# Optimization experiments

Hardware: AMD Instinct MI355X
Metric: run time of the kernel (lower is better)

The kernel has to match this reference:

```python
import jax, jax.numpy as jnp
import numpy as np

T, E, B, D, N = 4, 4096, 2, 128, 384


def setup_inputs() -> dict:
    key = jax.random.key(0)
    ks = jax.random.split(key, 8)
    x = jax.random.normal(ks[0], (T, E, B, D), jnp.float32)
    feats = jax.random.normal(ks[1], (N, N, B, D), jnp.float32)
    # Node ids in [1, N]; id 0 is the padding row/col of the (N+1,N+1) grid.
    # Shared edge list across the batch (matches the repo's usage: the torch
    # scatter broadcasts one value over all batch slots, which is only
    # self-consistent when nodes are identical across batch).
    nodes1 = jax.random.randint(ks[2], (1, E, 2), 1, N + 1)
    nodes = jnp.broadcast_to(nodes1, (B, E, 2)).astype(jnp.int32)
    padding_mask = jnp.zeros((B, E), bool)
    padding_mask_feats = jnp.zeros((B, N), bool)
    pad = jax.random.normal(ks[3], (1,), jnp.float32)
    s1 = 1.0 / np.sqrt(D)
    s2 = 1.0 / np.sqrt(2 * D)
    W_g = jax.random.normal(ks[4], (D, D), jnp.float32) * s1
    b_g = jnp.zeros((D,), jnp.float32)
    W_lin = jax.random.normal(ks[5], (D, 2 * D), jnp.float32) * s2
    b_lin = jnp.zeros((D,), jnp.float32)
    W_f = jax.random.normal(ks[6], (D, D), jnp.float32) * s1
    b_f = jnp.zeros((D,), jnp.float32)
    return dict(x=x, feats=feats, nodes=nodes, padding_mask=padding_mask,
                padding_mask_feats=padding_mask_feats, pad=pad,
                W_g=W_g, b_g=b_g, W_lin=W_lin, b_lin=b_lin, W_f=W_f, b_f=b_f)


def _forward(x, feats, nodes, pad, W_g, b_g, W_lin, b_lin, W_f, b_f):
    # graph_layer stand-in: dense projection over embed dim
    x = jnp.einsum('tebd,od->tebo', x, W_g) + b_g            # (T,E,B,D)
    n_nodes, _, bsz, dim = feats.shape
    xmean = x.mean(0)                                        # (E,B,D)
    # dense padded (N+1,N+1,B,D) grid filled with learned pad value (faithful)
    grid = jnp.ones((n_nodes + 1, n_nodes + 1, bsz, dim), x.dtype) * pad
    n0 = nodes[0, :, 0]                                      # (E,) shared graph
    n1 = nodes[0, :, 1]
    grid = grid.at[n0, n1].set(xmean)                        # scatter edges into grid
    feats_update = grid[1:, 1:]                              # drop pad row/col -> (N,N,B,D)
    cat = jnp.concatenate([feats, feats_update], axis=-1)    # (N,N,B,2D)
    feats = jnp.einsum('nmbc,oc->nmbo', cat, W_lin) + b_lin  # Linear(2D -> D)
    # feat_layer stand-in: dense projection
    feats = jnp.einsum('nmbd,od->nmbo', feats, W_f) + b_f
    nodes_0 = jnp.maximum(nodes - 1, 0)                      # clamp after -1 shift
    g0 = nodes_0[:, :, 0].T                                  # (E,B)
    g1 = nodes_0[:, :, 1].T
    bidx = jnp.arange(bsz)[None, :]                          # (1,B)
    feats_subset = feats[g0, g1, bidx]                       # gather -> (E,B,D)
    x = x + feats_subset[None]                               # broadcast over trials
    return x, feats


def reference(x, feats, nodes, padding_mask, padding_mask_feats, pad,
              W_g, b_g, W_lin, b_lin, W_f, b_f):
    # padding masks are accepted for signature parity; the stub sub-layers
    # (single linear projections) do not consume them.
    return _forward(x, feats, nodes, pad, W_g, b_g, W_lin, b_lin, W_f, b_f)
```

## Files before the change

### kernel.cpp

```cpp
#include <hip/hip_runtime.h>
#include <hip/hip_bf16.h>


constexpr int T_ = 4, E_ = 4096, B_ = 2, D_ = 128, N_ = 384;
constexpr int EB = E_ * B_;
constexpr int XSTRIDE_T = E_ * B_ * D_;
constexpr int XROWS = T_ * EB;
constexpr int NROWS = N_ * N_ * B_;
constexpr int NCELLS = N_ * N_;

typedef __attribute__((ext_vector_type(8))) short bf16x8;
typedef __attribute__((ext_vector_type(4))) float f32x4;
union BF8 { bf16x8 v; ushort u[8]; };

constexpr size_t OFF_WTG    = 0;
constexpr size_t OFF_WTL    = 16384;
constexpr size_t OFF_WTR    = 32768;
constexpr size_t OFF_BCOMB  = 49152;
constexpr size_t OFF_BP     = 49280;
constexpr size_t OFF_XMEAN  = 49408;
constexpr size_t OFF_UC     = OFF_XMEAN + (size_t)EB * D_;
constexpr size_t OFF_WIN    = OFF_UC + (size_t)EB * D_;
constexpr size_t OFF_BPACK  = OFF_WIN + (size_t)NCELLS;
constexpr size_t OFF_BPACKG = OFF_BPACK + 16384;
constexpr size_t OFF_BPACKR = OFF_BPACKG + 16384;
constexpr size_t OFF_WGR    = OFF_BPACKR + 16384;
constexpr size_t OFF_BGR    = OFF_WGR + 16384;
constexpr size_t WS_FLOATS  = OFF_BGR + 128;

static __device__ inline ushort f2bf(float x) {
  const uint u = __float_as_uint(x);
  return (ushort)((u + 0x7fffu + ((u >> 16) & 1u)) >> 16);
}
static __device__ inline float bf2f(ushort h) {
  return __uint_as_float(((uint)h) << 16);
}

__global__ __launch_bounds__(256) void prep_kernel(
    const float* __restrict__ W_f, const float* __restrict__ W_lin,
    const float* __restrict__ W_g, const float* __restrict__ b_lin,
    const float* __restrict__ b_f, const float* __restrict__ pad,
    float* __restrict__ WtG, float* __restrict__ WtL, float* __restrict__ WtR,
    float* __restrict__ bcomb, float* __restrict__ bp, int* __restrict__ winner) {
  const int o = blockIdx.x;
  const int c = threadIdx.x;

  for (int i = blockIdx.x * 256 + c; i < NCELLS; i += 128 * 256) winner[i] = -1;

  float acc = 0.f;
#pragma unroll 4
  for (int d = 0; d < D_; ++d) acc += W_f[o * D_ + d] * W_lin[d * (2 * D_) + c];

  if (c < D_) {
    WtL[c * D_ + o] = acc;
    WtG[c * D_ + o] = W_g[o * D_ + c];
  } else {
    WtR[(c - D_) * D_ + o] = acc;
  }

  __shared__ float red[256];
  red[c] = (c >= D_) ? acc : 0.f;
  __syncthreads();
  for (int s = 128; s > 0; s >>= 1) {
    if (c < s) red[c] += red[c + s];
    __syncthreads();
  }
  const float padsum = red[0];
  __syncthreads();
  red[c] = (c < D_) ? W_f[o * D_ + c] * b_lin[c] : 0.f;
  __syncthreads();
  for (int s = 128; s > 0; s >>= 1) {
    if (c < s) red[c] += red[c + s];
    __syncthreads();
  }
  if (c == 0) {
    const float bc = b_f[o] + red[0];
    bcomb[o] = bc;
    bp[o] = bc + pad[0] * padsum;
  }
}

__global__ __launch_bounds__(128) void prepB_kernel(
    const float* __restrict__ WtR, const float* __restrict__ W_g,
    const float* __restrict__ b_g, float* __restrict__ Wgr_kn,
    float* __restrict__ bgr) {
  const int o = blockIdx.x;
  const int c = threadIdx.x;
  float acc = 0.f;
#pragma unroll 4
  for (int d = 0; d < D_; ++d) acc += WtR[d * D_ + o] * W_g[d * D_ + c];
  Wgr_kn[c * D_ + o] = acc;

  __shared__ float red[128];
  red[c] = WtR[c * D_ + o] * b_g[c];
  __syncthreads();
  for (int s = 64; s > 0; s >>= 1) {
    if (c < s) red[c] += red[c + s];
    __syncthreads();
  }
  if (c == 0) bgr[o] = red[0];
}

__global__ __launch_bounds__(64) void prep2_kernel(
    const float* __restrict__ Wkn, ushort* __restrict__ Bpack) {
  const int fi = blockIdx.x;
  const int l = threadIdx.x;
  const int ishi = (fi >> 5) ^ 1;
  const int k0 = (fi >> 3) & 3;
  const int n0 = fi & 7;
  const int o = n0 * 16 + (l & 15);
  const int kb = k0 * 32 + ((l >> 4) & 3) * 8;
  ushort* dst = Bpack + ((size_t)fi * 64 + l) * 8;
#pragma unroll
  for (int j = 0; j < 8; ++j) {
    const float w = Wkn[(size_t)(kb + j) * D_ + o];
    const ushort h = f2bf(w);
    if (ishi) {
      dst[j] = h;
    } else {
      dst[j] = f2bf(w - bf2f(h));
    }
  }
}

__global__ __launch_bounds__(256) void scatter_kernel(
    const int* __restrict__ nodes, int* __restrict__ winner) {
  const int e = blockIdx.x * 256 + threadIdx.x;
  if (e < E_) {
    const int n0 = nodes[e * 2 + 0];
    const int n1 = nodes[e * 2 + 1];
    atomicMax(&winner[(n0 - 1) * N_ + (n1 - 1)], e);
  }
}

__global__ __launch_bounds__(256) void tile_mfma_kernel(
    const float* __restrict__ A, const ushort* __restrict__ Bpack,
    const float* __restrict__ bias, float* __restrict__ out, int ntiles) {
  __shared__ float lA[64 * 128];
  __shared__ bf16x8 lBhi[2048];
  const int tid = threadIdx.x;
  const int stride = gridDim.x;

  {
    const bf16x8* src = (const bf16x8*)Bpack;
    for (int i = tid; i < 2048; i += 256) lBhi[i] = src[i];
  }

  const int wave = tid >> 6, lane = tid & 63;
  const int l15 = lane & 15;
  const int lh = (lane >> 4) & 3;
  const int arow = wave * 16 + l15;
  const int asw = (arow & 7) << 2;
  const bf16x8* __restrict__ bp8 = (const bf16x8*)Bpack;

  float bs8[8];
#pragma unroll
  for (int n0 = 0; n0 < 8; ++n0) bs8[n0] = bias ? bias[n0 * 16 + l15] : 0.f;

  int tile = blockIdx.x;
  float4 pf[8];
  if (tile < ntiles) {
    const size_t t0 = (size_t)tile * 64;
#pragma unroll
    for (int j = 0; j < 8; ++j) {
      const int idx = j * 256 + tid;
      pf[j] = *(const float4*)&A[(t0 + (idx >> 5)) * D_ + (idx & 31) * 4];
    }
  }

  for (; tile < ntiles; tile += stride) {
    const size_t tile0 = (size_t)tile * 64;
    __syncthreads();
#pragma unroll
    for (int j = 0; j < 8; ++j) {
      const int idx = j * 256 + tid;
      const int row = idx >> 5, c4 = idx & 31;
      *(float4*)&lA[(row * 128 + c4 * 4) ^ ((row & 7) << 2)] = pf[j];
    }
    __syncthreads();

    const int next = tile + stride;
    if (next < ntiles) {
      const size_t t0 = (size_t)next * 64;
#pragma unroll
      for (int j = 0; j < 8; ++j) {
        const int idx = j * 256 + tid;
        pf[j] = *(const float4*)&A[(t0 + (idx >> 5)) * D_ + (idx & 31) * 4];
      }
    }

    f32x4 acc[8];
#pragma unroll
    for (int n0 = 0; n0 < 8; ++n0) {
      acc[n0][0] = bs8[n0]; acc[n0][1] = bs8[n0];
      acc[n0][2] = bs8[n0]; acc[n0][3] = bs8[n0];
    }

#pragma unroll
    for (int k0 = 0; k0 < 4; ++k0) {
      bf16x8 bl[8];
#pragma unroll
      for (int n0 = 0; n0 < 8; ++n0)
        bl[n0] = bp8[(size_t)((32 + k0 * 8 + n0) * 64 + lane)];
      const int base = arow * 128 + lh * 8 + k0 * 32;
      const float4 a0 = *(const float4*)&lA[(base + 0) ^ asw];
      const float4 a1 = *(const float4*)&lA[(base + 4) ^ asw];
      const float xs[8] = {a0.x, a0.y, a0.z, a0.w, a1.x, a1.y, a1.z, a1.w};
      BF8 ah, al;
#pragma unroll
      for (int j = 0; j < 8; ++j) {
        const ushort h = f2bf(xs[j]);
        ah.u[j] = h;
        al.u[j] = f2bf(xs[j] - bf2f(h));
      }
      bf16x8 bh[8];
#pragma unroll
      for (int n0 = 0; n0 < 8; ++n0)
        bh[n0] = lBhi[(k0 * 8 + n0) * 64 + lane];
#pragma unroll
      for (int n0 = 0; n0 < 8; ++n0) {
        acc[n0] = __builtin_amdgcn_mfma_f32_16x16x32_bf16(ah.v, bh[n0], acc[n0], 0, 0, 0);
        acc[n0] = __builtin_amdgcn_mfma_f32_16x16x32_bf16(al.v, bh[n0], acc[n0], 0, 0, 0);
      }
#pragma unroll
      for (int n0 = 0; n0 < 8; ++n0)
        acc[n0] = __builtin_amdgcn_mfma_f32_16x16x32_bf16(ah.v, bl[n0], acc[n0], 0, 0, 0);
    }

    __syncthreads();
#pragma unroll
    for (int n0 = 0; n0 < 8; ++n0) {
      const int col = n0 * 16 + l15;
#pragma unroll
      for (int i = 0; i < 4; ++i) {
        const int row = wave * 16 + lh * 4 + i;
        lA[(row * 128 + col) ^ ((row & 7) << 2)] = acc[n0][i];
      }
    }
    __syncthreads();
#pragma unroll
    for (int j = 0; j < 8; ++j) {
      const int idx = j * 256 + tid;
      const int row = idx >> 5, c4 = idx & 31;
      const float4 v =
          *(const float4*)&lA[(row * 128 + c4 * 4) ^ ((row & 7) << 2)];
      *(float4*)&out[(tile0 + row) * D_ + c4 * 4] = v;
    }
  }
}

__global__ __launch_bounds__(256) void mean_kernel(
    const float* __restrict__ x, float* __restrict__ xmean) {
  const int idx = blockIdx.x * 256 + threadIdx.x;
  const int pair = idx >> 5;
  const int o4 = (idx & 31) * 4;
  const size_t base = (size_t)pair * D_ + o4;
  float4 s = *(const float4*)&x[base];
  const float4 v1 = *(const float4*)&x[base + (size_t)1 * XSTRIDE_T];
  const float4 v2 = *(const float4*)&x[base + (size_t)2 * XSTRIDE_T];
  const float4 v3 = *(const float4*)&x[base + (size_t)3 * XSTRIDE_T];
  s.x = (s.x + v1.x + v2.x + v3.x) * 0.25f;
  s.y = (s.y + v1.y + v2.y + v3.y) * 0.25f;
  s.z = (s.z + v1.z + v2.z + v3.z) * 0.25f;
  s.w = (s.w + v1.w + v2.w + v3.w) * 0.25f;
  *(float4*)&xmean[base] = s;
}

__global__ __launch_bounds__(256) void fixup_kernel(
    const int* __restrict__ nodes, const int* __restrict__ winner,
    const float* __restrict__ uc, const float* __restrict__ bcomb,
    const float* __restrict__ bp, float* __restrict__ out_feats) {
  const int e = blockIdx.x;
  const int n0 = nodes[e * 2 + 0] - 1;
  const int n1 = nodes[e * 2 + 1] - 1;
  const int cell = n0 * N_ + n1;
  if (winner[cell] != e) return;
  const int t = threadIdx.x;
  const int b = t >> 7, o = t & 127;
  out_feats[((size_t)cell * 2 + b) * D_ + o] +=
      uc[((size_t)e * 2 + b) * D_ + o] + bcomb[o] - bp[o];
}

__global__ __launch_bounds__(256) void gather_add_kernel(
    const int* __restrict__ nodes, const float* __restrict__ out_feats,
    float* __restrict__ out_x) {
  const int e = blockIdx.x;
  const int tid = threadIdx.x;
  const int b = tid >> 7, o = tid & 127;
  const int n0 = nodes[((size_t)b * E_ + e) * 2 + 0] - 1;
  const int n1 = nodes[((size_t)b * E_ + e) * 2 + 1] - 1;
  const float fs = out_feats[(((size_t)n0 * N_ + n1) * B_ + b) * D_ + o];
#pragma unroll
  for (int t = 0; t < T_; ++t)
    out_x[(((size_t)t * E_ + e) * B_ + b) * D_ + o] += fs;
}

extern "C" void kernel_launch(void* const* d_in, const int* in_sizes, int n_in,
                              void* d_out, int out_size, void* d_ws, size_t ws_size,
                              hipStream_t stream) {
  const float* x      = (const float*)d_in[0];
  const float* feats  = (const float*)d_in[1];
  const int*   nodes  = (const int*)d_in[2];
  const float* pad    = (const float*)d_in[5];
  const float* W_g    = (const float*)d_in[6];
  const float* b_g    = (const float*)d_in[7];
  const float* W_lin  = (const float*)d_in[8];
  const float* b_lin  = (const float*)d_in[9];
  const float* W_f    = (const float*)d_in[10];
  const float* b_f    = (const float*)d_in[11];

  float* out_x     = (float*)d_out;
  float* out_feats = out_x + (size_t)T_ * E_ * B_ * D_;

  if (ws_size < WS_FLOATS * sizeof(float) + 16) return;

  float*  wsf    = (float*)d_ws;
  float*  WtG    = wsf + OFF_WTG;
  float*  WtL    = wsf + OFF_WTL;
  float*  WtR    = wsf + OFF_WTR;
  float*  bcomb  = wsf + OFF_BCOMB;
  float*  bpv    = wsf + OFF_BP;
  float*  xmean  = wsf + OFF_XMEAN;
  float*  uc     = wsf + OFF_UC;
  int*    win    = (int*)(wsf + OFF_WIN);
  ushort* Bpack  = (ushort*)(wsf + OFF_BPACK);
  ushort* BpackG = (ushort*)(wsf + OFF_BPACKG);
  ushort* BpackR = (ushort*)(wsf + OFF_BPACKR);
  float*  WgrKn  = wsf + OFF_WGR;
  float*  bgr    = wsf + OFF_BGR;

  prep_kernel<<<dim3(128), dim3(256), 0, stream>>>(W_f, W_lin, W_g, b_lin, b_f,
                                                   pad, WtG, WtL, WtR, bcomb,
                                                   bpv, win);
  prepB_kernel<<<dim3(128), dim3(128), 0, stream>>>(WtR, W_g, b_g, WgrKn, bgr);
  prep2_kernel<<<dim3(64), dim3(64), 0, stream>>>(WtL, Bpack);
  prep2_kernel<<<dim3(64), dim3(64), 0, stream>>>(WtG, BpackG);
  prep2_kernel<<<dim3(64), dim3(64), 0, stream>>>(WgrKn, BpackR);
  scatter_kernel<<<dim3(E_ / 256), dim3(256), 0, stream>>>(nodes, win);
  mean_kernel<<<dim3(EB * 32 / 256), dim3(256), 0, stream>>>(x, xmean);

  tile_mfma_kernel<<<dim3(512), dim3(256), 0, stream>>>(x, BpackG, b_g, out_x,
                                                        XROWS / 64);
  tile_mfma_kernel<<<dim3(128), dim3(256), 0, stream>>>(xmean, BpackR, bgr, uc,
                                                        EB / 64);
  tile_mfma_kernel<<<dim3(512), dim3(256), 0, stream>>>(feats, Bpack, bpv,
                                                        out_feats, NROWS / 64);
  fixup_kernel<<<dim3(E_), dim3(256), 0, stream>>>(nodes, win, uc, bcomb, bpv,
                                                   out_feats);
  gather_add_kernel<<<dim3(E_), dim3(256), 0, stream>>>(nodes, out_feats,
                                                        out_x);
}
```

Baseline: 482.6 us.

## Fuse three GEMM launches into one persistent per-wave MFMA kernel

```diff
diff --git a/kernel.cpp b/kernel.cpp
--- a/kernel.cpp
+++ b/kernel.cpp
@@ -8,6 +8,11 @@
 constexpr int XROWS = T_ * EB;
 constexpr int NROWS = N_ * N_ * B_;
 constexpr int NCELLS = N_ * N_;
+
+constexpr int WT0 = XROWS / 16;
+constexpr int WT1 = EB / 16;
+constexpr int WT2 = NROWS / 16;
+constexpr int WTOT = WT0 + WT1 + WT2;
 
 typedef __attribute__((ext_vector_type(8))) short bf16x8;
 typedef __attribute__((ext_vector_type(4))) float f32x4;
@@ -102,7 +107,11 @@
 }
 
 __global__ __launch_bounds__(64) void prep2_kernel(
-    const float* __restrict__ Wkn, ushort* __restrict__ Bpack) {
+    const float* __restrict__ W0, const float* __restrict__ W1,
+    const float* __restrict__ W2, ushort* __restrict__ B0,
+    ushort* __restrict__ B1, ushort* __restrict__ B2) {
+  const float* Wkn = blockIdx.y == 0 ? W0 : (blockIdx.y == 1 ? W1 : W2);
+  ushort* Bpack    = blockIdx.y == 0 ? B0 : (blockIdx.y == 1 ? B1 : B2);
   const int fi = blockIdx.x;
   const int l = threadIdx.x;
   const int ishi = (fi >> 5) ^ 1;
@@ -130,122 +139,6 @@
     const int n0 = nodes[e * 2 + 0];
     const int n1 = nodes[e * 2 + 1];
     atomicMax(&winner[(n0 - 1) * N_ + (n1 - 1)], e);
-  }
-}
-
-__global__ __launch_bounds__(256) void tile_mfma_kernel(
-    const float* __restrict__ A, const ushort* __restrict__ Bpack,
-    const float* __restrict__ bias, float* __restrict__ out, int ntiles) {
-  __shared__ float lA[64 * 128];
-  __shared__ bf16x8 lBhi[2048];
-  const int tid = threadIdx.x;
-  const int stride = gridDim.x;
-
-  {
-    const bf16x8* src = (const bf16x8*)Bpack;
-    for (int i = tid; i < 2048; i += 256) lBhi[i] = src[i];
-  }
-
-  const int wave = tid >> 6, lane = tid & 63;
-  const int l15 = lane & 15;
-  const int lh = (lane >> 4) & 3;
-  const int arow = wave * 16 + l15;
-  const int asw = (arow & 7) << 2;
-  const bf16x8* __restrict__ bp8 = (const bf16x8*)Bpack;
-
-  float bs8[8];
-#pragma unroll
-  for (int n0 = 0; n0 < 8; ++n0) bs8[n0] = bias ? bias[n0 * 16 + l15] : 0.f;
-
-  int tile = blockIdx.x;
-  float4 pf[8];
-  if (tile < ntiles) {
-    const size_t t0 = (size_t)tile * 64;
-#pragma unroll
-    for (int j = 0; j < 8; ++j) {
-      const int idx = j * 256 + tid;
-      pf[j] = *(const float4*)&A[(t0 + (idx >> 5)) * D_ + (idx & 31) * 4];
-    }
-  }
-
-  for (; tile < ntiles; tile += stride) {
-    const size_t tile0 = (size_t)tile * 64;
-    __syncthreads();
-#pragma unroll
-    for (int j = 0; j < 8; ++j) {
-      const int idx = j * 256 + tid;
-      const int row = idx >> 5, c4 = idx & 31;
-      *(float4*)&lA[(row * 128 + c4 * 4) ^ ((row & 7) << 2)] = pf[j];
-    }
-    __syncthreads();
-
-    const int next = tile + stride;
-    if (next < ntiles) {
-      const size_t t0 = (size_t)next * 64;
-#pragma unroll
-      for (int j = 0; j < 8; ++j) {
-        const int idx = j * 256 + tid;
-        pf[j] = *(const float4*)&A[(t0 + (idx >> 5)) * D_ + (idx & 31) * 4];
-      }
-    }
-
-    f32x4 acc[8];
-#pragma unroll
-    for (int n0 = 0; n0 < 8; ++n0) {
-      acc[n0][0] = bs8[n0]; acc[n0][1] = bs8[n0];
-      acc[n0][2] = bs8[n0]; acc[n0][3] = bs8[n0];
-    }
-
-#pragma unroll
-    for (int k0 = 0; k0 < 4; ++k0) {
-      bf16x8 bl[8];
-#pragma unroll
-      for (int n0 = 0; n0 < 8; ++n0)
-        bl[n0] = bp8[(size_t)((32 + k0 * 8 + n0) * 64 + lane)];
-      const int base = arow * 128 + lh * 8 + k0 * 32;
-      const float4 a0 = *(const float4*)&lA[(base + 0) ^ asw];
-      const float4 a1 = *(const float4*)&lA[(base + 4) ^ asw];
-      const float xs[8] = {a0.x, a0.y, a0.z, a0.w, a1.x, a1.y, a1.z, a1.w};
-      BF8 ah, al;
-#pragma unroll
-      for (int j = 0; j < 8; ++j) {
-        const ushort h = f2bf(xs[j]);
-        ah.u[j] = h;
-        al.u[j] = f2bf(xs[j] - bf2f(h));
-      }
-      bf16x8 bh[8];
-#pragma unroll
-      for (int n0 = 0; n0 < 8; ++n0)
-        bh[n0] = lBhi[(k0 * 8 + n0) * 64 + lane];
-#pragma unroll
-      for (int n0 = 0; n0 < 8; ++n0) {
-        acc[n0] = __builtin_amdgcn_mfma_f32_16x16x32_bf16(ah.v, bh[n0], acc[n0], 0, 0, 0);
-        acc[n0] = __builtin_amdgcn_mfma_f32_16x16x32_bf16(al.v, bh[n0], acc[n0], 0, 0, 0);
-      }
-#pragma unroll
-      for (int n0 = 0; n0 < 8; ++n0)
-        acc[n0] = __builtin_amdgcn_mfma_f32_16x16x32_bf16(ah.v, bl[n0], acc[n0], 0, 0, 0);
-    }
-
-    __syncthreads();
-#pragma unroll
-    for (int n0 = 0; n0 < 8; ++n0) {
-      const int col = n0 * 16 + l15;
-#pragma unroll
-      for (int i = 0; i < 4; ++i) {
-        const int row = wave * 16 + lh * 4 + i;
-        lA[(row * 128 + col) ^ ((row & 7) << 2)] = acc[n0][i];
-      }
-    }
-    __syncthreads();
-#pragma unroll
-    for (int j = 0; j < 8; ++j) {
-      const int idx = j * 256 + tid;
-      const int row = idx >> 5, c4 = idx & 31;
-      const float4 v =
-          *(const float4*)&lA[(row * 128 + c4 * 4) ^ ((row & 7) << 2)];
-      *(float4*)&out[(tile0 + row) * D_ + c4 * 4] = v;
-    }
   }
 }
 
@@ -266,6 +159,119 @@
   *(float4*)&xmean[base] = s;
 }
 
+__global__ __launch_bounds__(256) void mega_mfma_kernel(
+    const float* __restrict__ x, const float* __restrict__ xmean,
+    const float* __restrict__ feats,
+    const ushort* __restrict__ BpG, const ushort* __restrict__ BpR,
+    const ushort* __restrict__ BpL,
+    const float* __restrict__ b_g, const float* __restrict__ bgr,
+    const float* __restrict__ bpv,
+    float* __restrict__ out_x, float* __restrict__ ucv,
+    float* __restrict__ out_feats) {
+  __shared__ float lw[4 * 2048];
+  const int tid = threadIdx.x;
+  const int wave = tid >> 6, lane = tid & 63;
+  float* __restrict__ wlds = lw + wave * 2048;
+  const int l15 = lane & 15;
+  const int lh = (lane >> 4) & 3;
+  const int asw = (l15 & 7) << 2;
+  const int NW = gridDim.x * 4;
+
+  int t = blockIdx.x * 4 + wave;
+  float4 pf[8];
+  {
+    const float* As; int r0;
+    if (t < WT0)            { As = x;     r0 = t * 16; }
+    else if (t < WT0 + WT1) { As = xmean; r0 = (t - WT0) * 16; }
+    else                    { As = feats; r0 = (t - WT0 - WT1) * 16; }
+#pragma unroll
+    for (int j = 0; j < 8; ++j) {
+      const int idx = j * 64 + lane;
+      pf[j] = *(const float4*)&As[((size_t)r0 + (idx >> 5)) * D_ + (idx & 31) * 4];
+    }
+  }
+
+  for (; t < WTOT; t += NW) {
+    const ushort* Bp; const float* bias; float* Dst; int r0;
+    if (t < WT0)            { Bp = BpG; bias = b_g; Dst = out_x;     r0 = t * 16; }
+    else if (t < WT0 + WT1) { Bp = BpR; bias = bgr; Dst = ucv;       r0 = (t - WT0) * 16; }
+    else                    { Bp = BpL; bias = bpv; Dst = out_feats; r0 = (t - WT0 - WT1) * 16; }
+
+#pragma unroll
+    for (int j = 0; j < 8; ++j) {
+      const int idx = j * 64 + lane;
+      const int row = idx >> 5, c4 = idx & 31;
+      *(float4*)&wlds[(row * 128 + c4 * 4) ^ ((row & 7) << 2)] = pf[j];
+    }
+
+    const int t2 = t + NW;
+    if (t2 < WTOT) {
+      const float* As; int r2;
+      if (t2 < WT0)            { As = x;     r2 = t2 * 16; }
+      else if (t2 < WT0 + WT1) { As = xmean; r2 = (t2 - WT0) * 16; }
+      else                     { As = feats; r2 = (t2 - WT0 - WT1) * 16; }
+#pragma unroll
+      for (int j = 0; j < 8; ++j) {
+        const int idx = j * 64 + lane;
+        pf[j] = *(const float4*)&As[((size_t)r2 + (idx >> 5)) * D_ + (idx & 31) * 4];
+      }
+    }
+
+    f32x4 acc[8];
+#pragma unroll
+    for (int n0 = 0; n0 < 8; ++n0) {
+      const float b = bias[n0 * 16 + l15];
+      acc[n0][0] = b; acc[n0][1] = b; acc[n0][2] = b; acc[n0][3] = b;
+    }
+
+    const bf16x8* __restrict__ bp8 = (const bf16x8*)Bp;
+#pragma unroll
+    for (int k0 = 0; k0 < 4; ++k0) {
+      bf16x8 bh[8], bl[8];
+#pragma unroll
+      for (int n0 = 0; n0 < 8; ++n0) {
+        bh[n0] = bp8[(size_t)((k0 * 8 + n0) * 64 + lane)];
+        bl[n0] = bp8[(size_t)((32 + k0 * 8 + n0) * 64 + lane)];
+      }
+      const int base = l15 * 128 + lh * 8 + k0 * 32;
+      const float4 a0 = *(const float4*)&wlds[(base + 0) ^ asw];
+      const float4 a1 = *(const float4*)&wlds[(base + 4) ^ asw];
+      const float xs[8] = {a0.x, a0.y, a0.z, a0.w, a1.x, a1.y, a1.z, a1.w};
+      BF8 ah, al;
+#pragma unroll
+      for (int j = 0; j < 8; ++j) {
+        const ushort h = f2bf(xs[j]);
+        ah.u[j] = h;
+        al.u[j] = f2bf(xs[j] - bf2f(h));
+      }
+#pragma unroll
+      for (int n0 = 0; n0 < 8; ++n0) {
+        acc[n0] = __builtin_amdgcn_mfma_f32_16x16x32_bf16(ah.v, bh[n0], acc[n0], 0, 0, 0);
+        acc[n0] = __builtin_amdgcn_mfma_f32_16x16x32_bf16(al.v, bh[n0], acc[n0], 0, 0, 0);
+        acc[n0] = __builtin_amdgcn_mfma_f32_16x16x32_bf16(ah.v, bl[n0], acc[n0], 0, 0, 0);
+      }
+    }
+
+#pragma unroll
+    for (int n0 = 0; n0 < 8; ++n0) {
+      const int col = n0 * 16 + l15;
+#pragma unroll
+      for (int i = 0; i < 4; ++i) {
+        const int row = lh * 4 + i;
+        wlds[(row * 128 + col) ^ ((row & 7) << 2)] = acc[n0][i];
+      }
+    }
+#pragma unroll
+    for (int j = 0; j < 8; ++j) {
+      const int idx = j * 64 + lane;
+      const int row = idx >> 5, c4 = idx & 31;
+      const float4 v =
+          *(const float4*)&wlds[(row * 128 + c4 * 4) ^ ((row & 7) << 2)];
+      *(float4*)&Dst[((size_t)r0 + row) * D_ + c4 * 4] = v;
+    }
+  }
+}
+
 __global__ __launch_bounds__(256) void fixup_kernel(
     const int* __restrict__ nodes, const int* __restrict__ winner,
     const float* __restrict__ uc, const float* __restrict__ bcomb,
@@ -333,18 +339,14 @@
                                                    pad, WtG, WtL, WtR, bcomb,
                                                    bpv, win);
   prepB_kernel<<<dim3(128), dim3(128), 0, stream>>>(WtR, W_g, b_g, WgrKn, bgr);
-  prep2_kernel<<<dim3(64), dim3(64), 0, stream>>>(WtL, Bpack);
-  prep2_kernel<<<dim3(64), dim3(64), 0, stream>>>(WtG, BpackG);
-  prep2_kernel<<<dim3(64), dim3(64), 0, stream>>>(WgrKn, BpackR);
+  prep2_kernel<<<dim3(64, 3), dim3(64), 0, stream>>>(WtL, WtG, WgrKn, Bpack,
+                                                     BpackG, BpackR);
   scatter_kernel<<<dim3(E_ / 256), dim3(256), 0, stream>>>(nodes, win);
   mean_kernel<<<dim3(EB * 32 / 256), dim3(256), 0, stream>>>(x, xmean);
 
-  tile_mfma_kernel<<<dim3(512), dim3(256), 0, stream>>>(x, BpackG, b_g, out_x,
-                                                        XROWS / 64);
-  tile_mfma_kernel<<<dim3(128), dim3(256), 0, stream>>>(xmean, BpackR, bgr, uc,
-                                                        EB / 64);
-  tile_mfma_kernel<<<dim3(512), dim3(256), 0, stream>>>(feats, Bpack, bpv,
-                                                        out_feats, NROWS / 64);
+  mega_mfma_kernel<<<dim3(1024), dim3(256), 0, stream>>>(
+      x, xmean, feats, BpackG, BpackR, Bpack, b_g, bgr, bpv, out_x, uc,
+      out_feats);
   fixup_kernel<<<dim3(E_), dim3(256), 0, stream>>>(nodes, win, uc, bcomb, bpv,
                                                    out_feats);
   gather_add_kernel<<<dim3(E_), dim3(256), 0, stream>>>(nodes, out_feats,
```

New measurement: 443.8 us. 1.09x faster.
